# Optimization experiments

Measured on AMD Instinct MI355X. Metric: run time of the kernel, lower is better.

Reference implementation:

```python
import jax, jax.numpy as jnp
import numpy as np

N = 100000      # num_nodes
E = 6400000     # num edges
D = 128         # embedding_dim
R = 8           # num_roles
ALPHA = 0.15
ITERS = 10

def setup_inputs() -> dict:
    key = jax.random.key(0)
    k1, k2, k3, k4, k5 = jax.random.split(key, 5)
    edge_index = jax.random.randint(k1, (2, E), 0, N)
    batch_nodes = jax.random.randint(k2, (N,), 0, N)
    importance_emb = jax.random.normal(k3, (N, D), dtype=jnp.float32)
    resizer_W = jax.random.normal(k4, (D, 2), dtype=jnp.float32) * (1.0 / np.sqrt(D))
    resizer_b = jnp.zeros((2,), dtype=jnp.float32)
    # xavier_uniform for behavior_matrix [R, 4]
    limit = np.sqrt(6.0 / (R + 4))
    behavior_matrix = jax.random.uniform(k5, (R, 4), minval=-limit, maxval=limit, dtype=jnp.float32)
    return {
        'edge_index': edge_index,
        'batch_nodes': batch_nodes,
        'importance_emb': importance_emb,
        'resizer_W': resizer_W,
        'resizer_b': resizer_b,
        'behavior_matrix': behavior_matrix,
    }

def reference(edge_index, batch_nodes, importance_emb, resizer_W, resizer_b, behavior_matrix):
    src, dst = edge_index[0], edge_index[1]
    num_edges = src.shape[0]
    # out-degrees via segment_sum (== bincount)
    out_deg = jax.ops.segment_sum(jnp.ones((num_edges,), jnp.float32), src, num_segments=N)
    inv_deg_src = 1.0 / jnp.maximum(out_deg, 1.0)[src]  # [E], clamp(min=1)

    # approximate_pagerank: 10 iterations of gather -> scale -> scatter_add
    def body(pr, _):
        contrib = (1.0 - ALPHA) * pr[src] * inv_deg_src
        new_pr = jax.ops.segment_sum(contrib, dst, num_segments=N) + ALPHA / N
        return new_pr, None
    pr0 = jnp.full((N,), 1.0 / N, dtype=jnp.float32)
    pagerank, _ = jax.lax.scan(body, pr0, None, length=ITERS)

    # resizer: single Linear(D, 2)
    emb2 = importance_emb @ resizer_W + resizer_b  # [B, 2]

    # X = [deg[batch], pagerank[batch], emb2] -> [B, 4]
    X = jnp.concatenate([out_deg[batch_nodes][:, None],
                         pagerank[batch_nodes][:, None],
                         emb2], axis=1)

    # lstsq(H.T, X.T): A = H.T is [4, R], underdetermined -> minimum-norm
    # solution Z = A^T (A A^T)^{-1} X^T ; W = Z^T  -> [B, R]
    A = behavior_matrix.T                      # [4, R]
    G = A @ A.T                                # [4, 4]
    W = (A.T @ jnp.linalg.solve(G, X.T)).T     # [B, R]

    # F.normalize(W, p=2, dim=1)
    norm = jnp.linalg.norm(W, axis=1, keepdims=True)
    roles = W / jnp.maximum(norm, 1e-12)
    return roles
```

## Files before the change

kernel.cpp:

```cpp
#include <hip/hip_runtime.h>
#include <math.h>

#define N_NODES 100000
#define N_EDGES 6400000
#define DIM     128
#define NROLES  8
#define ALPHA   0.15f
#define PR_ITERS 10

#define DSH      8
#define DBS      256
#define NDB      391
#define SSH      9
#define SBS      512
#define NSB      196
#define NBT      587
#define NBLK_BIN 512
#define CHUNK    12500
#define SEG      4
#define CAPS     17408

__global__ __launch_bounds__(256)
void k_hist(const int* __restrict__ src, const int* __restrict__ dst,
            unsigned* __restrict__ counts) {
    __shared__ unsigned h[NBT];
    for (int i = threadIdx.x; i < NBT; i += 256) h[i] = 0;
    __syncthreads();
    int beg = blockIdx.x * CHUNK;
    int t = threadIdx.x;
    int mainEnd = beg + 12288;
    for (int e = beg + t * 4; e < mainEnd; e += 1024) {
        int4 s4 = *(const int4*)(src + e);
        int4 d4 = *(const int4*)(dst + e);
        atomicAdd(&h[((unsigned)d4.x) >> DSH], 1u);
        atomicAdd(&h[((unsigned)d4.y) >> DSH], 1u);
        atomicAdd(&h[((unsigned)d4.z) >> DSH], 1u);
        atomicAdd(&h[((unsigned)d4.w) >> DSH], 1u);
        atomicAdd(&h[NDB + (((unsigned)s4.x) >> SSH)], 1u);
        atomicAdd(&h[NDB + (((unsigned)s4.y) >> SSH)], 1u);
        atomicAdd(&h[NDB + (((unsigned)s4.z) >> SSH)], 1u);
        atomicAdd(&h[NDB + (((unsigned)s4.w) >> SSH)], 1u);
    }
    for (int e = mainEnd + t; e < beg + CHUNK; e += 256) {
        atomicAdd(&h[((unsigned)dst[e]) >> DSH], 1u);
        atomicAdd(&h[NDB + (((unsigned)src[e]) >> SSH)], 1u);
    }
    __syncthreads();
    for (int i = threadIdx.x; i < NBT; i += 256)
        counts[blockIdx.x * NBT + i] = h[i];
}

__global__ __launch_bounds__(512)
void k_scanA(const unsigned* __restrict__ counts, unsigned* __restrict__ offs,
             unsigned* __restrict__ btot) {
    int bucket = blockIdx.x, t = threadIdx.x, lane = t & 63, wv = t >> 6;
    unsigned v = counts[t * NBT + bucket], x = v;
    #pragma unroll
    for (int o = 1; o < 64; o <<= 1) {
        unsigned y = __shfl_up(x, o);
        if (lane >= o) x += y;
    }
    __shared__ unsigned wsum[8];
    if (lane == 63) wsum[wv] = x;
    __syncthreads();
    unsigned carry = 0;
    for (int w = 0; w < wv; ++w) carry += wsum[w];
    x += carry;
    offs[t * NBT + bucket] = x - v;
    if (t == 511) btot[bucket] = x;
}

__global__ __launch_bounds__(512)
void k_scanB(const unsigned* __restrict__ btot, unsigned* __restrict__ bases,
             const float* __restrict__ H, float* __restrict__ Mout) {
    if (blockIdx.x == 2) {
        if (threadIdx.x != 0) return;
        double G[4][4];
        for (int i = 0; i < 4; ++i)
            for (int j = 0; j < 4; ++j) {
                double s = 0.0;
                for (int r = 0; r < NROLES; ++r)
                    s += (double)H[r * 4 + i] * (double)H[r * 4 + j];
                G[i][j] = s;
            }
        double aug[4][8];
        for (int i = 0; i < 4; ++i)
            for (int j = 0; j < 4; ++j) {
                aug[i][j] = G[i][j];
                aug[i][j + 4] = (i == j) ? 1.0 : 0.0;
            }
        for (int c = 0; c < 4; ++c) {
            int p = c; double best = fabs(aug[c][c]);
            for (int r = c + 1; r < 4; ++r) {
                double v = fabs(aug[r][c]);
                if (v > best) { best = v; p = r; }
            }
            if (p != c)
                for (int j = 0; j < 8; ++j) {
                    double tt = aug[c][j]; aug[c][j] = aug[p][j]; aug[p][j] = tt;
                }
            double piv = aug[c][c];
            for (int j = 0; j < 8; ++j) aug[c][j] /= piv;
            for (int r = 0; r < 4; ++r) {
                if (r == c) continue;
                double f = aug[r][c];
                for (int j = 0; j < 8; ++j) aug[r][j] -= f * aug[c][j];
            }
        }
        for (int r = 0; r < NROLES; ++r)
            for (int k = 0; k < 4; ++k) {
                double s = 0.0;
                for (int j = 0; j < 4; ++j)
                    s += (double)H[r * 4 + j] * aug[j][k + 4];
                Mout[r * 4 + k] = (float)s;
            }
        return;
    }
    int half = blockIdx.x;
    int len  = half ? NSB : NDB;
    int t = threadIdx.x, lane = t & 63, wv = t >> 6;
    unsigned v = (t < len) ? btot[(half ? NDB : 0) + t] : 0u, x = v;
    #pragma unroll
    for (int o = 1; o < 64; o <<= 1) {
        unsigned y = __shfl_up(x, o);
        if (lane >= o) x += y;
    }
    __shared__ unsigned wsum[8];
    if (lane == 63) wsum[wv] = x;
    __syncthreads();
    unsigned carry = 0;
    for (int w = 0; w < wv; ++w) carry += wsum[w];
    x += carry;
    if (t <= len) bases[half * 512 + t] = x - v;
}

__global__ __launch_bounds__(512)
void k_place(const int* __restrict__ src, const int* __restrict__ dst,
             const unsigned* __restrict__ counts, const unsigned* __restrict__ offs,
             const unsigned* __restrict__ bases,
             unsigned* __restrict__ rec, unsigned short* __restrict__ recs) {
    __shared__ unsigned buf[CHUNK];
    __shared__ unsigned loc[NDB + 1];
    __shared__ unsigned cur[NDB];
    __shared__ unsigned wsum[8];
    int t = threadIdx.x, lane = t & 63, wv = t >> 6;
    int blk = blockIdx.x;
    int beg = blk * CHUNK;
    int mainEnd = beg + 12288;

    {
        unsigned c = (t < NDB) ? counts[blk * NBT + t] : 0u;
        unsigned x = c;
        #pragma unroll
        for (int o = 1; o < 64; o <<= 1) {
            unsigned y = __shfl_up(x, o);
            if (lane >= o) x += y;
        }
        if (lane == 63) wsum[wv] = x;
        __syncthreads();
        unsigned carry = 0;
        for (int w = 0; w < wv; ++w) carry += wsum[w];
        x += carry;
        if (t < NDB) { loc[t] = x - c; cur[t] = x - c; }
        if (t == NDB - 1) loc[NDB] = x;
    }
    __syncthreads();
    for (int e = beg + t * 4; e < mainEnd; e += 2048) {
        int4 s4 = *(const int4*)(src + e);
        int4 d4 = *(const int4*)(dst + e);
        #pragma unroll
        for (int k = 0; k < 4; ++k) {
            unsigned s = (unsigned)((&s4.x)[k]);
            unsigned d = (unsigned)((&d4.x)[k]);
            unsigned p = atomicAdd(&cur[d >> DSH], 1u);
            buf[p] = ((d & (DBS - 1)) << 17) | s;
        }
    }
    for (int e = mainEnd + t; e < beg + CHUNK; e += 512) {
        unsigned s = (unsigned)src[e];
        unsigned d = (unsigned)dst[e];
        unsigned p = atomicAdd(&cur[d >> DSH], 1u);
        buf[p] = ((d & (DBS - 1)) << 17) | s;
    }
    __syncthreads();
    for (int i = wv; i < NDB; i += 8) {
        unsigned lo = loc[i], n = loc[i + 1] - lo;
        unsigned gbase = bases[i] + offs[blk * NBT + i];
        for (unsigned j = lane; j < n; j += 64)
            rec[gbase + j] = buf[lo + j];
    }
    __syncthreads();

    {
        unsigned c = (t < NSB) ? counts[blk * NBT + NDB + t] : 0u;
        unsigned x = c;
        #pragma unroll
        for (int o = 1; o < 64; o <<= 1) {
            unsigned y = __shfl_up(x, o);
            if (lane >= o) x += y;
        }
        if (lane == 63) wsum[wv] = x;
        __syncthreads();
        unsigned carry = 0;
        for (int w = 0; w < wv; ++w) carry += wsum[w];
        x += carry;
        if (t < NSB) { loc[t] = x - c; cur[t] = x - c; }
        if (t == NSB - 1) loc[NSB] = x;
    }
    __syncthreads();
    unsigned short* b16 = (unsigned short*)buf;
    for (int e = beg + t * 4; e < mainEnd; e += 2048) {
        int4 s4 = *(const int4*)(src + e);
        #pragma unroll
        for (int k = 0; k < 4; ++k) {
            unsigned s = (unsigned)((&s4.x)[k]);
            unsigned p = atomicAdd(&cur[s >> SSH], 1u);
            b16[p] = (unsigned short)(s & (SBS - 1));
        }
    }
    for (int e = mainEnd + t; e < beg + CHUNK; e += 512) {
        unsigned s = (unsigned)src[e];
        unsigned p = atomicAdd(&cur[s >> SSH], 1u);
        b16[p] = (unsigned short)(s & (SBS - 1));
    }
    __syncthreads();
    for (int i = wv; i < NSB; i += 8) {
        unsigned lo = loc[i], n = loc[i + 1] - lo;
        unsigned gbase = bases[512 + i] + offs[blk * NBT + NDB + i];
        for (unsigned j = lane; j < n; j += 64)
            recs[gbase + j] = b16[lo + j];
    }
}

__global__ __launch_bounds__(256)
void k_count_init(const unsigned short* __restrict__ recs,
                  const unsigned* __restrict__ bases,
                  float* __restrict__ deg, float* __restrict__ s,
                  float* __restrict__ val0) {
    __shared__ unsigned cnt[SBS];
    int t = threadIdx.x;
    cnt[t] = 0; cnt[t + 256] = 0;
    __syncthreads();
    int b = blockIdx.x;
    unsigned st = bases[512 + b], en = bases[512 + b + 1];
    unsigned a = (st + 7u) & ~7u;
    if (a > en) a = en;
    for (unsigned i = st + t; i < a; i += 256)
        atomicAdd(&cnt[recs[i]], 1u);
    unsigned mainN = (en - a) & ~2047u;
    const uint4* rp = (const uint4*)(recs + a);
    for (unsigned i = t; i * 8u < mainN; i += 256) {
        uint4 r = rp[i];
        atomicAdd(&cnt[r.x & 0xFFFFu], 1u); atomicAdd(&cnt[r.x >> 16], 1u);
        atomicAdd(&cnt[r.y & 0xFFFFu], 1u); atomicAdd(&cnt[r.y >> 16], 1u);
        atomicAdd(&cnt[r.z & 0xFFFFu], 1u); atomicAdd(&cnt[r.z >> 16], 1u);
        atomicAdd(&cnt[r.w & 0xFFFFu], 1u); atomicAdd(&cnt[r.w >> 16], 1u);
    }
    for (unsigned i = a + mainN + t; i < en; i += 256)
        atomicAdd(&cnt[recs[i]], 1u);
    __syncthreads();
    #pragma unroll
    for (int k = 0; k < 2; ++k) {
        int v = b * SBS + t + k * 256;
        if (v < N_NODES) {
            float d = (float)cnt[t + k * 256];
            float sv = (1.0f - ALPHA) / fmaxf(d, 1.0f);
            deg[v] = d;
            s[v] = sv;
            val0[v] = sv * (1.0f / (float)N_NODES);
        }
    }
}

__global__ __launch_bounds__(256)
void k_sortD(const unsigned* __restrict__ rec, const unsigned* __restrict__ bases,
             unsigned* __restrict__ rec2) {
    __shared__ unsigned hist[DBS];
    __shared__ unsigned wsum[4];
    __shared__ unsigned buf[CAPS];
    int t = threadIdx.x, lane = t & 63, wv = t >> 6;
    int b = blockIdx.x;
    unsigned st = bases[b], en = bases[b + 1], n = en - st;
    if (n > CAPS) {
        for (unsigned i = st + t; i < en; i += 256) rec2[i] = rec[i];
        return;
    }
    hist[t] = 0;
    __syncthreads();
    for (unsigned i = st + t; i < en; i += 256)
        atomicAdd(&hist[rec[i] >> 17], 1u);
    __syncthreads();
    unsigned c = hist[t], x = c;
    #pragma unroll
    for (int o = 1; o < 64; o <<= 1) {
        unsigned y = __shfl_up(x, o);
        if (lane >= o) x += y;
    }
    if (lane == 63) wsum[wv] = x;
    __syncthreads();
    unsigned carry = 0;
    for (int w = 0; w < wv; ++w) carry += wsum[w];
    x += carry;
    hist[t] = x - c;
    __syncthreads();
    for (unsigned i = st + t; i < en; i += 256) {
        unsigned r = rec[i];
        unsigned p = atomicAdd(&hist[r >> 17], 1u);
        buf[p] = r;
    }
    __syncthreads();
    for (unsigned i = t; i < n; i += 256) rec2[st + i] = buf[i];
}

__global__ __launch_bounds__(256)
void k_iterD(const unsigned* __restrict__ rec2, const unsigned* __restrict__ bases,
             const float* __restrict__ val, float* __restrict__ partial) {
    __shared__ float acc[DBS];
    int t = threadIdx.x, lane = t & 63;
    int b = blockIdx.x >> 2, seg = blockIdx.x & 3;
    acc[t] = 0.0f;
    __syncthreads();
    unsigned st = bases[b], en = bases[b + 1], n = en - st;
    unsigned s0 = st + (unsigned)(((unsigned long long)n * (unsigned)seg) >> 2);
    unsigned s1 = st + (unsigned)(((unsigned long long)n * (unsigned)(seg + 1)) >> 2);
    for (unsigned base = s0; base < s1; base += 256) {
        unsigned i = base + t;
        bool ok = (i < s1);
        unsigned r = ok ? rec2[i] : 0xFFFFFFFFu;
        float v = ok ? val[r & 0x1FFFFu] : 0.0f;
        unsigned k = r >> 17;
        unsigned kp = __shfl_up(k, 1);
        bool head = (lane == 0) || (kp != k);
        unsigned long long hmask = __ballot(head);
        float x = v;
        #pragma unroll
        for (int off = 1; off < 64; off <<= 1) {
            float y = __shfl_up(x, off);
            if (lane >= off) x += y;
        }
        unsigned long long le = (~0ull) >> (63 - lane);
        int H = 63 - __clzll(hmask & le);
        float prev = __shfl(x, H - 1);
        float runsum = x - ((H == 0) ? 0.0f : prev);
        bool tail = (lane == 63) || (((hmask >> lane) >> 1) & 1ull);
        if (tail && ok) atomicAdd(&acc[k], runsum);
    }
    __syncthreads();
    partial[((unsigned)blockIdx.x << 8) + t] = acc[t];
}

__global__ __launch_bounds__(256)
void k_reduceS(const float* __restrict__ partial, const float* __restrict__ s,
               float* __restrict__ pr, float* __restrict__ valn) {
    int v = blockIdx.x * 256 + threadIdx.x;
    if (v >= N_NODES) return;
    unsigned b = (unsigned)v >> DSH;
    int local = v & (DBS - 1);
    const float* p = partial + ((b * SEG) << 8) + local;
    float sum = p[0] + p[256] + p[512] + p[768];
    float pv = sum + ALPHA / (float)N_NODES;
    pr[v] = pv;
    valn[v] = pv * s[v];
}

__global__ __launch_bounds__(256)
void k_final(const float* __restrict__ emb, const float* __restrict__ rW,
             const float* __restrict__ rb, const int* __restrict__ batch,
             const float* __restrict__ deg, const float* __restrict__ pr,
             const float* __restrict__ M, float* __restrict__ out) {
    int wid  = (blockIdx.x * blockDim.x + threadIdx.x) >> 6;
    int lane = threadIdx.x & 63;
    if (wid >= N_NODES) return;

    const float* row = emb + (size_t)wid * DIM;
    float e0 = row[lane];
    float e1 = row[lane + 64];
    float2 w0 = ((const float2*)rW)[lane];
    float2 w1 = ((const float2*)rW)[lane + 64];
    float a0 = e0 * w0.x + e1 * w1.x;
    float a1 = e0 * w0.y + e1 * w1.y;
    #pragma unroll
    for (int off = 32; off; off >>= 1) {
        a0 += __shfl_xor(a0, off);
        a1 += __shfl_xor(a1, off);
    }

    int bn = batch[wid];
    float x0 = deg[bn];
    float x1 = pr[bn];
    float x2 = a0 + rb[0];
    float x3 = a1 + rb[1];

    float wr = 0.0f;
    if (lane < NROLES) {
        const float* m = M + lane * 4;
        wr = m[0] * x0 + m[1] * x1 + m[2] * x2 + m[3] * x3;
    }
    float sq = wr * wr;
    #pragma unroll
    for (int off = 4; off; off >>= 1) sq += __shfl_xor(sq, off);
    float inv = 1.0f / fmaxf(sqrtf(sq), 1e-12f);
    if (lane < NROLES) out[(size_t)wid * NROLES + lane] = wr * inv;
}

extern "C" void kernel_launch(void* const* d_in, const int* in_sizes, int n_in,
                              void* d_out, int out_size, void* d_ws, size_t ws_size,
                              hipStream_t stream) {
    const int*   edge  = (const int*)d_in[0];
    const int*   src   = edge;
    const int*   dst   = edge + N_EDGES;
    const int*   batch = (const int*)d_in[1];
    const float* emb   = (const float*)d_in[2];
    const float* rW    = (const float*)d_in[3];
    const float* rb    = (const float*)d_in[4];
    const float* H     = (const float*)d_in[5];
    float*       out   = (float*)d_out;

    float*    deg    = (float*)d_ws;
    float*    s      = deg   + 100352;
    float*    pr     = s     + 100352;
    float*    valA   = pr    + 100352;
    float*    valB   = valA  + 100352;
    float*    M      = valB  + 100352;
    unsigned* counts = (unsigned*)(M + 32);
    unsigned* offs   = counts + NBLK_BIN * NBT;
    unsigned* btot   = offs   + NBLK_BIN * NBT;
    unsigned* bases  = btot   + 1024;
    unsigned* rec    = bases  + 1024;
    unsigned* rec2   = rec    + N_EDGES;
    unsigned short* recs = (unsigned short*)rec2;
    float*    partial = (float*)(rec2 + N_EDGES);

    k_hist <<<NBLK_BIN, 256, 0, stream>>>(src, dst, counts);
    k_scanA<<<NBT,      512, 0, stream>>>(counts, offs, btot);
    k_scanB<<<3,        512, 0, stream>>>(btot, bases, H, M);
    k_place<<<NBLK_BIN, 512, 0, stream>>>(src, dst, counts, offs, bases, rec, recs);
    k_count_init<<<NSB, 256, 0, stream>>>(recs, bases, deg, s, valA);
    k_sortD<<<NDB,      256, 0, stream>>>(rec, bases, rec2);

    float* vcur = valA;
    float* vnxt = valB;
    for (int it = 0; it < PR_ITERS; ++it) {
        k_iterD <<<NDB * SEG, 256, 0, stream>>>(rec2, bases, vcur, partial);
        k_reduceS<<<NDB, 256, 0, stream>>>(partial, s, pr, vnxt);
        float* t = vcur; vcur = vnxt; vnxt = t;
    }

    const int FG = (N_NODES + 3) / 4;
    k_final<<<FG, 256, 0, stream>>>(emb, rW, rb, batch, deg, pr, M, out);
}
```

Baseline: 463.5 us.

## Build per-node CSR row offsets and replace segmented-scan iteration with row gather

The destination-bucket sort now also emits per-node row offsets, which gives a CSR layout. Each PageRank iteration becomes a single kernel in which four lanes per node sum their slice of incoming contributions and combine the partial sums with shuffles. This removes the warp-level segmented scan, the shared-memory atomics, the partial-buffer write and the separate reduce kernel launched on every iteration. In exchange, load balance now depends on per-node degree, and the rare oversized buckets are sorted with global scatter writes instead of being copied through unsorted.

```diff
diff --git a/kernel.cpp b/kernel.cpp
--- a/kernel.cpp
+++ b/kernel.cpp
@@ -17,8 +17,9 @@
 #define NBT      587
 #define NBLK_BIN 512
 #define CHUNK    12500
-#define SEG      4
-#define CAPS     17408
+#define CAPS     18432
+#define SPLIT    4
+#define ITC_BLK  1563
 
 __global__ __launch_bounds__(256)
 void k_hist(const int* __restrict__ src, const int* __restrict__ dst,
@@ -274,17 +275,13 @@
 
 __global__ __launch_bounds__(256)
 void k_sortD(const unsigned* __restrict__ rec, const unsigned* __restrict__ bases,
-             unsigned* __restrict__ rec2) {
+             unsigned* __restrict__ rec2, unsigned* __restrict__ rowoff) {
     __shared__ unsigned hist[DBS];
     __shared__ unsigned wsum[4];
     __shared__ unsigned buf[CAPS];
     int t = threadIdx.x, lane = t & 63, wv = t >> 6;
     int b = blockIdx.x;
     unsigned st = bases[b], en = bases[b + 1], n = en - st;
-    if (n > CAPS) {
-        for (unsigned i = st + t; i < en; i += 256) rec2[i] = rec[i];
-        return;
-    }
     hist[t] = 0;
     __syncthreads();
     for (unsigned i = st + t; i < en; i += 256)
@@ -301,66 +298,58 @@
     unsigned carry = 0;
     for (int w = 0; w < wv; ++w) carry += wsum[w];
     x += carry;
-    hist[t] = x - c;
-    __syncthreads();
-    for (unsigned i = st + t; i < en; i += 256) {
-        unsigned r = rec[i];
-        unsigned p = atomicAdd(&hist[r >> 17], 1u);
-        buf[p] = r;
-    }
-    __syncthreads();
-    for (unsigned i = t; i < n; i += 256) rec2[st + i] = buf[i];
+    unsigned excl = x - c;
+    rowoff[b * DBS + t] = st + excl;
+    if (b == NDB - 1 && t == 255) rowoff[NDB * DBS] = en;
+    hist[t] = excl;
+    __syncthreads();
+    if (n <= CAPS) {
+        for (unsigned i = st + t; i < en; i += 256) {
+            unsigned r = rec[i];
+            unsigned p = atomicAdd(&hist[r >> 17], 1u);
+            buf[p] = r;
+        }
+        __syncthreads();
+        for (unsigned i = t; i < n; i += 256) rec2[st + i] = buf[i];
+    } else {
+        for (unsigned i = st + t; i < en; i += 256) {
+            unsigned r = rec[i];
+            rec2[st + atomicAdd(&hist[r >> 17], 1u)] = r;
+        }
+    }
 }
 
 __global__ __launch_bounds__(256)
-void k_iterD(const unsigned* __restrict__ rec2, const unsigned* __restrict__ bases,
-             const float* __restrict__ val, float* __restrict__ partial) {
-    __shared__ float acc[DBS];
-    int t = threadIdx.x, lane = t & 63;
-    int b = blockIdx.x >> 2, seg = blockIdx.x & 3;
-    acc[t] = 0.0f;
-    __syncthreads();
-    unsigned st = bases[b], en = bases[b + 1], n = en - st;
-    unsigned s0 = st + (unsigned)(((unsigned long long)n * (unsigned)seg) >> 2);
-    unsigned s1 = st + (unsigned)(((unsigned long long)n * (unsigned)(seg + 1)) >> 2);
-    for (unsigned base = s0; base < s1; base += 256) {
-        unsigned i = base + t;
-        bool ok = (i < s1);
-        unsigned r = ok ? rec2[i] : 0xFFFFFFFFu;
-        float v = ok ? val[r & 0x1FFFFu] : 0.0f;
-        unsigned k = r >> 17;
-        unsigned kp = __shfl_up(k, 1);
-        bool head = (lane == 0) || (kp != k);
-        unsigned long long hmask = __ballot(head);
-        float x = v;
-        #pragma unroll
-        for (int off = 1; off < 64; off <<= 1) {
-            float y = __shfl_up(x, off);
-            if (lane >= off) x += y;
-        }
-        unsigned long long le = (~0ull) >> (63 - lane);
-        int H = 63 - __clzll(hmask & le);
-        float prev = __shfl(x, H - 1);
-        float runsum = x - ((H == 0) ? 0.0f : prev);
-        bool tail = (lane == 63) || (((hmask >> lane) >> 1) & 1ull);
-        if (tail && ok) atomicAdd(&acc[k], runsum);
-    }
-    __syncthreads();
-    partial[((unsigned)blockIdx.x << 8) + t] = acc[t];
-}
-
-__global__ __launch_bounds__(256)
-void k_reduceS(const float* __restrict__ partial, const float* __restrict__ s,
-               float* __restrict__ pr, float* __restrict__ valn) {
-    int v = blockIdx.x * 256 + threadIdx.x;
-    if (v >= N_NODES) return;
-    unsigned b = (unsigned)v >> DSH;
-    int local = v & (DBS - 1);
-    const float* p = partial + ((b * SEG) << 8) + local;
-    float sum = p[0] + p[256] + p[512] + p[768];
-    float pv = sum + ALPHA / (float)N_NODES;
-    pr[v] = pv;
-    valn[v] = pv * s[v];
+void k_iterC(const unsigned* __restrict__ rec2, const unsigned* __restrict__ rowoff,
+             const float* __restrict__ val, const float* __restrict__ s,
+             float* __restrict__ pr, float* __restrict__ valn) {
+    int g = blockIdx.x * 256 + threadIdx.x;
+    int v = g >> 2, q = g & 3;
+    if (v > N_NODES) return;
+    unsigned st = rowoff[v], en = rowoff[v + 1], n = en - st;
+    unsigned q0 = st + ((n * (unsigned)q) >> 2);
+    unsigned q1 = st + ((n * (unsigned)(q + 1)) >> 2);
+    float a0 = 0.0f, a1 = 0.0f, a2 = 0.0f, a3 = 0.0f;
+    unsigned i = q0;
+    for (; i + 4 <= q1; i += 4) {
+        unsigned r0 = rec2[i];
+        unsigned r1 = rec2[i + 1];
+        unsigned r2 = rec2[i + 2];
+        unsigned r3 = rec2[i + 3];
+        a0 += val[r0 & 0x1FFFFu];
+        a1 += val[r1 & 0x1FFFFu];
+        a2 += val[r2 & 0x1FFFFu];
+        a3 += val[r3 & 0x1FFFFu];
+    }
+    for (; i < q1; ++i) a0 += val[rec2[i] & 0x1FFFFu];
+    float sum = (a0 + a1) + (a2 + a3);
+    sum += __shfl_xor(sum, 1);
+    sum += __shfl_xor(sum, 2);
+    if (q == 0 && v < N_NODES) {
+        float pv = sum + ALPHA / (float)N_NODES;
+        pr[v] = pv;
+        valn[v] = pv * s[v];
+    }
 }
 
 __global__ __launch_bounds__(256)
@@ -429,20 +418,19 @@
     unsigned* rec    = bases  + 1024;
     unsigned* rec2   = rec    + N_EDGES;
     unsigned short* recs = (unsigned short*)rec2;
-    float*    partial = (float*)(rec2 + N_EDGES);
+    unsigned* rowoff = rec2 + N_EDGES;
 
     k_hist <<<NBLK_BIN, 256, 0, stream>>>(src, dst, counts);
     k_scanA<<<NBT,      512, 0, stream>>>(counts, offs, btot);
     k_scanB<<<3,        512, 0, stream>>>(btot, bases, H, M);
     k_place<<<NBLK_BIN, 512, 0, stream>>>(src, dst, counts, offs, bases, rec, recs);
     k_count_init<<<NSB, 256, 0, stream>>>(recs, bases, deg, s, valA);
-    k_sortD<<<NDB,      256, 0, stream>>>(rec, bases, rec2);
+    k_sortD<<<NDB,      256, 0, stream>>>(rec, bases, rec2, rowoff);
 
     float* vcur = valA;
     float* vnxt = valB;
     for (int it = 0; it < PR_ITERS; ++it) {
-        k_iterD <<<NDB * SEG, 256, 0, stream>>>(rec2, bases, vcur, partial);
-        k_reduceS<<<NDB, 256, 0, stream>>>(partial, s, pr, vnxt);
+        k_iterC<<<ITC_BLK, 256, 0, stream>>>(rec2, rowoff, vcur, s, pr, vnxt);
         float* t = vcur; vcur = vnxt; vnxt = t;
     }
 
```

New measurement: 487.3 us. 5.1% more time.
